# Performance work log

Hardware: AMD Instinct MI355X
Metric: run time of the kernel (lower is better)

## Reference

```python
import jax, jax.numpy as jnp
import numpy as np

ALPHA = 0.2  # LeakyReLU slope in GAT
OUT_SLOPE = 0.01  # default nn.LeakyyReLU slope for self.out
B, E, IN_DIM, HID, HEADS = 4, 2048, 32, 18, 3
DH = HID // HEADS  # per-head out dim = 6


def _leaky(x, slope):
    return jnp.where(x > 0, x, slope * x)


def _gat_head(x, adj, W, a):
    # x: [B,E,in], W: [in,dh], a: [2*dh,1]
    h = jnp.einsum('bei,id->bed', x, W)                      # [B,E,dh]
    d = h.shape[-1]
    # score[b,i,j] = leakyrelu(a . concat(h_i, h_j)) = leakyrelu(h_i.a1 + h_j.a2)
    e1 = jnp.einsum('bed,d->be', h, a[:d, 0])
    e2 = jnp.einsum('bed,d->be', h, a[d:, 0])
    score = _leaky(e1[:, :, None] + e2[:, None, :], ALPHA)   # [B,E,E]
    scores = jnp.where(adj == 1.0, score, 0.0)
    logits = jnp.where(adj > 0.0, scores, -30.0)
    att = jax.nn.softmax(logits, axis=2)                     # softmax over j
    # h_prime[b,j,d] = sum_i att[b,i,j] * h[b,i,d]  (torch sums over dim=1)
    h_prime = jnp.einsum('bij,bid->bjd', att, h)
    return jax.nn.elu(h_prime)  # concat=True -> elu


def _gat_multihead(x, adj, Ws, As):
    # Ws: [H,in,dh], As: [H,2*dh,1]
    outs = jax.vmap(lambda W, a: _gat_head(x, adj, W, a))(Ws, As)  # [H,B,E,dh]
    H, b, e, d = outs.shape
    return jnp.moveaxis(outs, 0, 2).reshape(b, e, H * d)  # concat heads last-dim


def _gcn(x, adj2d, W, b):
    return adj2d @ (x @ W) + b


def setup_inputs() -> dict:
    key = jax.random.key(0)
    ks = jax.random.split(key, 16)
    node_input = jax.random.normal(ks[0], (B, E, IN_DIM), jnp.float32)
    uv_filed = jax.random.normal(ks[1], (B, E, IN_DIM), jnp.float32)
    adj = jax.random.randint(ks[2], (B, E, E), 0, 2).astype(jnp.float32)
    s = 0.1
    Wt1 = jax.random.normal(ks[3], (HEADS, IN_DIM, DH), jnp.float32) * s
    at1 = jax.random.normal(ks[4], (HEADS, 2 * DH, 1), jnp.float32) * s
    Wt2 = jax.random.normal(ks[5], (HEADS, IN_DIM, DH), jnp.float32) * s
    at2 = jax.random.normal(ks[6], (HEADS, 2 * DH, 1), jnp.float32) * s
    Wg1 = jax.random.normal(ks[7], (HID, 16), jnp.float32) * s
    bg1 = jnp.zeros((16,), jnp.float32)
    Wg2 = jax.random.normal(ks[8], (16, 2), jnp.float32) * s
    bg2 = jnp.zeros((2,), jnp.float32)
    Wo1 = jax.random.normal(ks[9], (HID, 16), jnp.float32) * s
    bo1 = jnp.zeros((16,), jnp.float32)
    Wo2 = jax.random.normal(ks[10], (16, 2), jnp.float32) * s
    bo2 = jnp.zeros((2,), jnp.float32)
    return dict(node_input=node_input, uv_filed=uv_filed, adj=adj,
                Wt1=Wt1, at1=at1, Wt2=Wt2, at2=at2,
                Wg1=Wg1, bg1=bg1, Wg2=Wg2, bg2=bg2,
                Wo1=Wo1, bo1=bo1, Wo2=Wo2, bo2=bo2)


def reference(node_input, uv_filed, adj, Wt1, at1, Wt2, at2,
              Wg1, bg1, Wg2, bg2, Wo1, bo1, Wo2, bo2):
    h = _gat_multihead(node_input, adj, Wt1, at1)  # [B,E,18]
    o = _gat_multihead(uv_filed, adj, Wt2, at2)    # [B,E,18]
    a0 = adj[0]
    Y = jax.nn.relu(_gcn(h[0], a0, Wg1, bg1))
    O = jax.nn.relu(_gcn(o[0], a0, Wo1, bo1))
    Y = _gcn(Y, a0, Wg2, bg2)
    O = _gcn(O, a0, Wo2, bo2)
    return (jax.nn.log_softmax(Y, axis=1), _leaky(O, OUT_SLOPE))
```

## Files before the change

### kernel.cpp

```cpp
#include <hip/hip_runtime.h>
#include <hip/hip_bf16.h>


__global__ __launch_bounds__(256) void k0_bitmask(
    const float* __restrict__ adj0, unsigned int* __restrict__ bm) {
  int lane = threadIdx.x & 63, w = threadIdx.x >> 6;
  int row = blockIdx.x * 4 + w;
  const float* arow = adj0 + (size_t)row * 2048;
#pragma unroll 4
  for (int it = 0; it < 32; ++it) {
    float v = arow[it * 64 + lane];
    unsigned long long mask = __ballot(v == 1.0f);
    if (lane == 0) bm[row * 64 + it * 2] = (unsigned int)mask;
    else if (lane == 32) bm[row * 64 + it * 2 + 1] = (unsigned int)(mask >> 32);
  }
}

__global__ __launch_bounds__(256) void k1_features(
    const float* __restrict__ node, const float* __restrict__ uv,
    const float* __restrict__ Wt1, const float* __restrict__ at1,
    const float* __restrict__ Wt2, const float* __restrict__ at2,
    float* __restrict__ hcol, float* __restrict__ pack1, float* __restrict__ pack2) {
  __shared__ float sW[192];
  __shared__ float sA[12];
  int b = blockIdx.x;
  int g = b / 24;
  int h = (b / 8) % 3;
  int e = (b % 8) * 256 + threadIdx.x;
  const float* W = (g ? Wt2 : Wt1) + h * 192;
  const float* A = (g ? at2 : at1) + h * 12;
  const float* x = (g ? uv : node) + e * 32;
  if (threadIdx.x < 192) sW[threadIdx.x] = W[threadIdx.x];
  if (threadIdx.x < 12) sA[threadIdx.x] = A[threadIdx.x];
  __syncthreads();
  float xv[32];
#pragma unroll
  for (int i = 0; i < 32; ++i) xv[i] = x[i];
  float hv[6];
#pragma unroll
  for (int d = 0; d < 6; ++d) hv[d] = 0.f;
#pragma unroll
  for (int i = 0; i < 32; ++i)
#pragma unroll
    for (int d = 0; d < 6; ++d) hv[d] += xv[i] * sW[i * 6 + d];
  float e1 = 0.f, e2 = 0.f;
#pragma unroll
  for (int d = 0; d < 6; ++d) {
    e1 += hv[d] * sA[d];
    e2 += hv[d] * sA[6 + d];
  }
  int c = g * 3 + h;
#pragma unroll
  for (int d = 0; d < 6; ++d) hcol[(c * 6 + d) * 2048 + e] = hv[d];
  pack1[c * 2048 + e] = e1;
  pack1[(6 + c) * 2048 + e] = __expf(e1);
  pack1[(12 + c) * 2048 + e] = __expf(0.2f * e1);
  pack2[c * 2048 + e] = e2;
  pack2[(6 + c) * 2048 + e] = __expf(e2);
  pack2[(12 + c) * 2048 + e] = __expf(0.2f * e2);
}

__global__ __launch_bounds__(384) void k2_rowsum(
    const unsigned int* __restrict__ bm, const float* __restrict__ pack1,
    const float* __restrict__ pack2, float* __restrict__ invrs) {
  int tid = threadIdx.x;
  int c = tid >> 6, lane = tid & 63;
  int i0 = blockIdx.x * 8;
  const float4* p2_4 = (const float4*)pack2;
  float e1r[8], p1r[8], q1r[8], sum[8];
#pragma unroll
  for (int r = 0; r < 8; ++r) {
    e1r[r] = pack1[c * 2048 + i0 + r];
    p1r[r] = pack1[(6 + c) * 2048 + i0 + r];
    q1r[r] = pack1[(12 + c) * 2048 + i0 + r];
    sum[r] = 0.f;
  }
  int sh = (lane & 7) * 4;
#pragma unroll
  for (int it = 0; it < 8; ++it) {
    int j4 = it * 64 + lane;
    float4 e2 = p2_4[c * 512 + j4];
    float4 p2 = p2_4[(6 + c) * 512 + j4];
    float4 q2 = p2_4[(12 + c) * 512 + j4];
    int wbase = it * 8 + (lane >> 3);
    float abx, aby, abz, abw;
#pragma unroll
    for (int r = 0; r < 8; ++r) {
      unsigned int wd = bm[(i0 + r) * 64 + wbase] >> sh;
      { float e = e1r[r] + e2.x; bool p = e > 0.f;
        abx = (p ? p1r[r] : q1r[r]) * (p ? p2.x : q2.x); }
      { float e = e1r[r] + e2.y; bool p = e > 0.f;
        aby = (p ? p1r[r] : q1r[r]) * (p ? p2.y : q2.y); }
      { float e = e1r[r] + e2.z; bool p = e > 0.f;
        abz = (p ? p1r[r] : q1r[r]) * (p ? p2.z : q2.z); }
      { float e = e1r[r] + e2.w; bool p = e > 0.f;
        abw = (p ? p1r[r] : q1r[r]) * (p ? p2.w : q2.w); }
      float s = ((wd & 1u) ? abx : 0.f) + ((wd & 2u) ? aby : 0.f) +
                ((wd & 4u) ? abz : 0.f) + ((wd & 8u) ? abw : 0.f);
      sum[r] += s;
    }
  }
#pragma unroll
  for (int r = 0; r < 8; ++r) {
#pragma unroll
    for (int off = 32; off > 0; off >>= 1) sum[r] += __shfl_down(sum[r], off);
  }
  if (lane == 0) {
#pragma unroll
    for (int r = 0; r < 8; ++r) invrs[c * 2048 + i0 + r] = 1.0f / sum[r];
  }
}

__global__ __launch_bounds__(384) void k3_hprime(
    const unsigned int* __restrict__ bm, const float* __restrict__ hcol,
    const float* __restrict__ pack1, const float* __restrict__ pack2,
    const float* __restrict__ invrs, float* __restrict__ hp_part) {
  __shared__ float4 sPack[6 * 64];
  __shared__ float sHS[6 * 64 * 8];
  __shared__ unsigned int sM[64 * 4];
  float4* sHS4 = (float4*)sHS;
  int tid = threadIdx.x;
  int c6 = tid >> 6, jl = tid & 63;
  int j0 = blockIdx.x * 128;
  int jA = j0 + jl, jB = jA + 64;
  float e2A = pack2[c6 * 2048 + jA];
  float p2A = pack2[(6 + c6) * 2048 + jA];
  float q2A = pack2[(12 + c6) * 2048 + jA];
  float e2B = pack2[c6 * 2048 + jB];
  float p2B = pack2[(6 + c6) * 2048 + jB];
  float q2B = pack2[(12 + c6) * 2048 + jB];
  float aA0 = 0.f, aA1 = 0.f, aA2 = 0.f, aA3 = 0.f, aA4 = 0.f, aA5 = 0.f;
  float aB0 = 0.f, aB1 = 0.f, aB2 = 0.f, aB3 = 0.f, aB4 = 0.f, aB5 = 0.f;
  int hi = jl >> 5;
  int shj = jl & 31;
  int ibeg = blockIdx.y * 128;
  for (int i0 = ibeg; i0 < ibeg + 128; i0 += 64) {
    __syncthreads();
    {
      int cc = c6, ii = jl;
      float e1 = pack1[cc * 2048 + i0 + ii];
      float p1 = pack1[(6 + cc) * 2048 + i0 + ii];
      float q1 = pack1[(12 + cc) * 2048 + i0 + ii];
      sPack[cc * 64 + ii] = make_float4(e1, p1, q1, 0.f);
      float iv = invrs[cc * 2048 + i0 + ii];
#pragma unroll
      for (int d = 0; d < 6; ++d)
        sHS[(cc * 64 + ii) * 8 + d] = hcol[(cc * 6 + d) * 2048 + i0 + ii] * iv;
      sHS[(cc * 64 + ii) * 8 + 6] = 0.f;
      sHS[(cc * 64 + ii) * 8 + 7] = 0.f;
    }
    if (tid < 256) sM[tid] = bm[(size_t)(i0 + (tid >> 2)) * 64 + (j0 >> 5) + (tid & 3)];
    __syncthreads();
#pragma unroll 8
    for (int ii = 0; ii < 64; ++ii) {
      float4 pk = sPack[c6 * 64 + ii];
      float4 h0 = sHS4[(c6 * 64 + ii) * 2];
      float4 h1 = sHS4[(c6 * 64 + ii) * 2 + 1];
      unsigned int wdA = sM[ii * 4 + hi];
      unsigned int wdB = sM[ii * 4 + 2 + hi];
      {
        float e = pk.x + e2A; bool p = e > 0.f;
        float ab = (p ? pk.y : pk.z) * (p ? p2A : q2A);
        float wgt = ((wdA >> shj) & 1u) ? ab : 0.f;
        aA0 += wgt * h0.x; aA1 += wgt * h0.y; aA2 += wgt * h0.z;
        aA3 += wgt * h0.w; aA4 += wgt * h1.x; aA5 += wgt * h1.y;
      }
      {
        float e = pk.x + e2B; bool p = e > 0.f;
        float ab = (p ? pk.y : pk.z) * (p ? p2B : q2B);
        float wgt = ((wdB >> shj) & 1u) ? ab : 0.f;
        aB0 += wgt * h0.x; aB1 += wgt * h0.y; aB2 += wgt * h0.z;
        aB3 += wgt * h0.w; aB4 += wgt * h1.x; aB5 += wgt * h1.y;
      }
    }
  }
  float* hp = hp_part + (size_t)blockIdx.y * 73728;
  int kb = c6 * 6;
  hp[(kb + 0) * 2048 + jA] = aA0;
  hp[(kb + 1) * 2048 + jA] = aA1;
  hp[(kb + 2) * 2048 + jA] = aA2;
  hp[(kb + 3) * 2048 + jA] = aA3;
  hp[(kb + 4) * 2048 + jA] = aA4;
  hp[(kb + 5) * 2048 + jA] = aA5;
  hp[(kb + 0) * 2048 + jB] = aB0;
  hp[(kb + 1) * 2048 + jB] = aB1;
  hp[(kb + 2) * 2048 + jB] = aB2;
  hp[(kb + 3) * 2048 + jB] = aB3;
  hp[(kb + 4) * 2048 + jB] = aB4;
  hp[(kb + 5) * 2048 + jB] = aB5;
}

__global__ __launch_bounds__(256) void k4_T(
    const float* __restrict__ hp_part, const float* __restrict__ Wg1,
    const float* __restrict__ Wo1, float* __restrict__ T) {
  __shared__ float sHP[16 * 37];
  __shared__ float sWg[288], sWo[288];
  int tid = threadIdx.x;
  int j0 = blockIdx.x * 16;
  for (int idx = tid; idx < 288; idx += 256) {
    sWg[idx] = Wg1[idx];
    sWo[idx] = Wo1[idx];
  }
  for (int idx = tid; idx < 576; idx += 256) {
    int r = idx >> 4, jl = idx & 15;
    float s = 0.f;
#pragma unroll
    for (int sp = 0; sp < 16; ++sp)
      s += hp_part[(size_t)sp * 73728 + r * 2048 + j0 + jl];
    sHP[jl * 37 + r] = s;
  }
  __syncthreads();
  int jl = tid & 15, wq = tid >> 4;
  int gat = wq >> 3;
  int c0 = (wq & 7) * 2;
  const float* Wp = gat ? sWo : sWg;
  float a0 = 0.f, a1 = 0.f;
#pragma unroll
  for (int r = 0; r < 18; ++r) {
    float x = sHP[jl * 37 + gat * 18 + r];
    float hc = x > 0.f ? x : __expf(x) - 1.f;
    a0 += hc * Wp[r * 16 + c0];
    a1 += hc * Wp[r * 16 + c0 + 1];
  }
  T[(j0 + jl) * 32 + gat * 16 + c0] = a0;
  T[(j0 + jl) * 32 + gat * 16 + c0 + 1] = a1;
}

__global__ __launch_bounds__(256) void k5_gcn1(
    const unsigned int* __restrict__ bm, const float* __restrict__ T,
    float* __restrict__ Craw_part) {
  __shared__ unsigned int sM[64 * 4];
  __shared__ float4 sT4[128 * 8];
  const float4* T4 = (const float4*)T;
  int tid = threadIdx.x;
  int rl = tid & 31, cg = tid >> 5;
  int i0 = blockIdx.x * 64;
  int k0 = blockIdx.y * 128;
  if (tid < 256) sM[tid] = bm[(size_t)(i0 + (tid >> 2)) * 64 + (k0 >> 5) + (tid & 3)];
  for (int idx = tid; idx < 1024; idx += 256) sT4[idx] = T4[k0 * 8 + idx];
  __syncthreads();
  float a0x = 0.f, a0y = 0.f, a0z = 0.f, a0w = 0.f;
  float a1x = 0.f, a1y = 0.f, a1z = 0.f, a1w = 0.f;
#pragma unroll
  for (int wi = 0; wi < 4; ++wi) {
    unsigned int wA = sM[rl * 4 + wi];
    unsigned int wB = sM[(rl + 32) * 4 + wi];
#pragma unroll 16
    for (int kb = 0; kb < 32; ++kb) {
      float4 t = sT4[(wi * 32 + kb) * 8 + cg];
      float mA = (float)((wA >> kb) & 1u);
      float mB = (float)((wB >> kb) & 1u);
      a0x += mA * t.x; a0y += mA * t.y; a0z += mA * t.z; a0w += mA * t.w;
      a1x += mB * t.x; a1y += mB * t.y; a1z += mB * t.z; a1w += mB * t.w;
    }
  }
  float* base = Craw_part + (size_t)blockIdx.y * 65536;
  *(float4*)&base[(i0 + rl) * 32 + cg * 4] = make_float4(a0x, a0y, a0z, a0w);
  *(float4*)&base[(i0 + rl + 32) * 32 + cg * 4] = make_float4(a1x, a1y, a1z, a1w);
}

__global__ __launch_bounds__(256) void k6_T2(
    const float* __restrict__ Craw_part, const float* __restrict__ bg1,
    const float* __restrict__ Wg2, const float* __restrict__ bo1,
    const float* __restrict__ Wo2, float* __restrict__ T2) {
  int tid = threadIdx.x;
  int wave = tid >> 6, lane = tid & 63;
  int j = blockIdx.x * 8 + wave * 2 + (lane >> 5);
  int cl = lane & 31;
  int gat = cl >> 4, cc = cl & 15;
  float x = 0.f;
#pragma unroll
  for (int sp = 0; sp < 16; ++sp) x += Craw_part[(size_t)sp * 65536 + j * 32 + cl];
  x += gat ? bo1[cc] : bg1[cc];
  x = x > 0.f ? x : 0.f;
  float wa = gat ? Wo2[cc * 2 + 0] : Wg2[cc * 2 + 0];
  float wb = gat ? Wo2[cc * 2 + 1] : Wg2[cc * 2 + 1];
  float pa = x * wa, pb = x * wb;
#pragma unroll
  for (int m = 8; m > 0; m >>= 1) {
    pa += __shfl_xor(pa, m);
    pb += __shfl_xor(pb, m);
  }
  if (cc == 0) {
    T2[j * 4 + gat * 2 + 0] = pa;
    T2[j * 4 + gat * 2 + 1] = pb;
  }
}

__global__ __launch_bounds__(256) void k7_final(
    const unsigned int* __restrict__ bm, const float* __restrict__ T2,
    const float* __restrict__ bg2, const float* __restrict__ bo2,
    float* __restrict__ out) {
  int tid = threadIdx.x;
  int lane = tid & 63, w = tid >> 6;
  int r = blockIdx.x * 4 + w;
  const float4* T24 = (const float4*)T2;
  float4 acc = make_float4(0.f, 0.f, 0.f, 0.f);
  int sh = lane & 31;
#pragma unroll 8
  for (int it = 0; it < 32; ++it) {
    int k = it * 64 + lane;
    unsigned int wd = bm[r * 64 + it * 2 + (lane >> 5)];
    float m = (float)((wd >> sh) & 1u);
    float4 t = T24[k];
    acc.x += m * t.x;
    acc.y += m * t.y;
    acc.z += m * t.z;
    acc.w += m * t.w;
  }
#pragma unroll
  for (int off = 32; off > 0; off >>= 1) {
    acc.x += __shfl_down(acc.x, off);
    acc.y += __shfl_down(acc.y, off);
    acc.z += __shfl_down(acc.z, off);
    acc.w += __shfl_down(acc.w, off);
  }
  if (lane == 0) {
    float y0 = acc.x + bg2[0], y1 = acc.y + bg2[1];
    float m = fmaxf(y0, y1);
    float ls = m + logf(__expf(y0 - m) + __expf(y1 - m));
    out[r * 2 + 0] = y0 - ls;
    out[r * 2 + 1] = y1 - ls;
    float o0 = acc.z + bo2[0], o1 = acc.w + bo2[1];
    out[4096 + r * 2 + 0] = o0 > 0.f ? o0 : 0.01f * o0;
    out[4096 + r * 2 + 1] = o1 > 0.f ? o1 : 0.01f * o1;
  }
}

extern "C" void kernel_launch(void* const* d_in, const int* in_sizes, int n_in,
                              void* d_out, int out_size, void* d_ws, size_t ws_size,
                              hipStream_t stream) {
  const float* node = (const float*)d_in[0];
  const float* uv = (const float*)d_in[1];
  const float* adj = (const float*)d_in[2];
  const float* Wt1 = (const float*)d_in[3];
  const float* at1 = (const float*)d_in[4];
  const float* Wt2 = (const float*)d_in[5];
  const float* at2 = (const float*)d_in[6];
  const float* Wg1 = (const float*)d_in[7];
  const float* bg1 = (const float*)d_in[8];
  const float* Wg2 = (const float*)d_in[9];
  const float* bg2 = (const float*)d_in[10];
  const float* Wo1 = (const float*)d_in[11];
  const float* bo1 = (const float*)d_in[12];
  const float* Wo2 = (const float*)d_in[13];
  const float* bo2 = (const float*)d_in[14];
  float* ws = (float*)d_ws;
  float* hcol = ws;
  float* pack1 = ws + 73728;
  float* pack2 = ws + 110592;
  float* invrs = ws + 147456;
  float* T = ws + 159744;
  float* T2 = ws + 225280;
  unsigned int* bm = (unsigned int*)(ws + 233472);
  float* hp_part = ws + 364544;
  float* Craw_part = ws + 1544192;
  float* out = (float*)d_out;

  k0_bitmask<<<512, 256, 0, stream>>>(adj, bm);
  k1_features<<<48, 256, 0, stream>>>(node, uv, Wt1, at1, Wt2, at2, hcol, pack1, pack2);
  k2_rowsum<<<256, 384, 0, stream>>>(bm, pack1, pack2, invrs);
  k3_hprime<<<dim3(16, 16), 384, 0, stream>>>(bm, hcol, pack1, pack2, invrs, hp_part);
  k4_T<<<128, 256, 0, stream>>>(hp_part, Wg1, Wo1, T);
  k5_gcn1<<<dim3(32, 16), 256, 0, stream>>>(bm, T, Craw_part);
  k6_T2<<<256, 256, 0, stream>>>(Craw_part, bg1, Wg2, bo1, Wo2, T2);
  k7_final<<<512, 256, 0, stream>>>(bm, T2, bg2, bo2, out);
}
```

Measured before the change: 183.6 us.

## Merge bitmask and feature kernels, precompute scaled h, drop LDS staging in hprime

```diff
diff --git a/kernel.cpp b/kernel.cpp
--- a/kernel.cpp
+++ b/kernel.cpp
@@ -2,31 +2,32 @@
 #include <hip/hip_bf16.h>
 
 
-__global__ __launch_bounds__(256) void k0_bitmask(
-    const float* __restrict__ adj0, unsigned int* __restrict__ bm) {
-  int lane = threadIdx.x & 63, w = threadIdx.x >> 6;
-  int row = blockIdx.x * 4 + w;
-  const float* arow = adj0 + (size_t)row * 2048;
-#pragma unroll 4
-  for (int it = 0; it < 32; ++it) {
-    float v = arow[it * 64 + lane];
-    unsigned long long mask = __ballot(v == 1.0f);
-    if (lane == 0) bm[row * 64 + it * 2] = (unsigned int)mask;
-    else if (lane == 32) bm[row * 64 + it * 2 + 1] = (unsigned int)(mask >> 32);
-  }
-}
-
-__global__ __launch_bounds__(256) void k1_features(
+__global__ __launch_bounds__(256) void k01(
+    const float* __restrict__ adj0, unsigned int* __restrict__ bm,
     const float* __restrict__ node, const float* __restrict__ uv,
     const float* __restrict__ Wt1, const float* __restrict__ at1,
     const float* __restrict__ Wt2, const float* __restrict__ at2,
-    float* __restrict__ hcol, float* __restrict__ pack1, float* __restrict__ pack2) {
+    float* __restrict__ hcol, float4* __restrict__ pk1q, float* __restrict__ pack2) {
+  int b = blockIdx.x;
+  if (b < 512) {
+    int lane = threadIdx.x & 63, w = threadIdx.x >> 6;
+    int row = b * 4 + w;
+    const float* arow = adj0 + (size_t)row * 2048;
+#pragma unroll 4
+    for (int it = 0; it < 32; ++it) {
+      float v = arow[it * 64 + lane];
+      unsigned long long mask = __ballot(v == 1.0f);
+      if (lane == 0) bm[row * 64 + it * 2] = (unsigned int)mask;
+      else if (lane == 32) bm[row * 64 + it * 2 + 1] = (unsigned int)(mask >> 32);
+    }
+    return;
+  }
   __shared__ float sW[192];
   __shared__ float sA[12];
-  int b = blockIdx.x;
-  int g = b / 24;
-  int h = (b / 8) % 3;
-  int e = (b % 8) * 256 + threadIdx.x;
+  int fb = b - 512;
+  int g = fb / 24;
+  int h = (fb / 8) % 3;
+  int e = (fb % 8) * 256 + threadIdx.x;
   const float* W = (g ? Wt2 : Wt1) + h * 192;
   const float* A = (g ? at2 : at1) + h * 12;
   const float* x = (g ? uv : node) + e * 32;
@@ -52,27 +53,25 @@
   int c = g * 3 + h;
 #pragma unroll
   for (int d = 0; d < 6; ++d) hcol[(c * 6 + d) * 2048 + e] = hv[d];
-  pack1[c * 2048 + e] = e1;
-  pack1[(6 + c) * 2048 + e] = __expf(e1);
-  pack1[(12 + c) * 2048 + e] = __expf(0.2f * e1);
+  pk1q[c * 2048 + e] = make_float4(e1, __expf(e1), __expf(0.2f * e1), 0.f);
   pack2[c * 2048 + e] = e2;
   pack2[(6 + c) * 2048 + e] = __expf(e2);
   pack2[(12 + c) * 2048 + e] = __expf(0.2f * e2);
 }
 
-__global__ __launch_bounds__(384) void k2_rowsum(
-    const unsigned int* __restrict__ bm, const float* __restrict__ pack1,
-    const float* __restrict__ pack2, float* __restrict__ invrs) {
+__global__ __launch_bounds__(384) void k2_rowsum_hs(
+    const unsigned int* __restrict__ bm, const float4* __restrict__ pk1q,
+    const float* __restrict__ pack2, const float* __restrict__ hcol,
+    float* __restrict__ hs8) {
   int tid = threadIdx.x;
   int c = tid >> 6, lane = tid & 63;
-  int i0 = blockIdx.x * 8;
+  int i0 = blockIdx.x * 4;
   const float4* p2_4 = (const float4*)pack2;
-  float e1r[8], p1r[8], q1r[8], sum[8];
-#pragma unroll
-  for (int r = 0; r < 8; ++r) {
-    e1r[r] = pack1[c * 2048 + i0 + r];
-    p1r[r] = pack1[(6 + c) * 2048 + i0 + r];
-    q1r[r] = pack1[(12 + c) * 2048 + i0 + r];
+  float e1r[4], p1r[4], q1r[4], sum[4];
+#pragma unroll
+  for (int r = 0; r < 4; ++r) {
+    float4 pq = pk1q[c * 2048 + i0 + r];
+    e1r[r] = pq.x; p1r[r] = pq.y; q1r[r] = pq.z;
     sum[r] = 0.f;
   }
   int sh = (lane & 7) * 4;
@@ -85,7 +84,7 @@
     int wbase = it * 8 + (lane >> 3);
     float abx, aby, abz, abw;
 #pragma unroll
-    for (int r = 0; r < 8; ++r) {
+    for (int r = 0; r < 4; ++r) {
       unsigned int wd = bm[(i0 + r) * 64 + wbase] >> sh;
       { float e = e1r[r] + e2.x; bool p = e > 0.f;
         abx = (p ? p1r[r] : q1r[r]) * (p ? p2.x : q2.x); }
@@ -101,27 +100,29 @@
     }
   }
 #pragma unroll
-  for (int r = 0; r < 8; ++r) {
+  for (int r = 0; r < 4; ++r) {
 #pragma unroll
     for (int off = 32; off > 0; off >>= 1) sum[r] += __shfl_down(sum[r], off);
   }
-  if (lane == 0) {
-#pragma unroll
-    for (int r = 0; r < 8; ++r) invrs[c * 2048 + i0 + r] = 1.0f / sum[r];
+  float s0 = __shfl(sum[0], 0), s1 = __shfl(sum[1], 0);
+  float s2 = __shfl(sum[2], 0), s3 = __shfl(sum[3], 0);
+  if (lane < 32) {
+    int r = lane >> 3, d = lane & 7;
+    float sv = (r == 0) ? s0 : (r == 1) ? s1 : (r == 2) ? s2 : s3;
+    float v = 0.f;
+    if (d < 6) v = hcol[(c * 6 + d) * 2048 + i0 + r] * (1.0f / sv);
+    hs8[((size_t)c * 2048 + i0 + r) * 8 + d] = v;
   }
 }
 
 __global__ __launch_bounds__(384) void k3_hprime(
-    const unsigned int* __restrict__ bm, const float* __restrict__ hcol,
-    const float* __restrict__ pack1, const float* __restrict__ pack2,
-    const float* __restrict__ invrs, float* __restrict__ hp_part) {
-  __shared__ float4 sPack[6 * 64];
-  __shared__ float sHS[6 * 64 * 8];
-  __shared__ unsigned int sM[64 * 4];
-  float4* sHS4 = (float4*)sHS;
+    const unsigned int* __restrict__ bm, const float4* __restrict__ pk1q,
+    const float* __restrict__ pack2, const float4* __restrict__ hs8,
+    float* __restrict__ hp_part) {
   int tid = threadIdx.x;
   int c6 = tid >> 6, jl = tid & 63;
   int j0 = blockIdx.x * 128;
+  int i0 = blockIdx.y * 64;
   int jA = j0 + jl, jB = jA + 64;
   float e2A = pack2[c6 * 2048 + jA];
   float p2A = pack2[(6 + c6) * 2048 + jA];
@@ -133,45 +134,30 @@
   float aB0 = 0.f, aB1 = 0.f, aB2 = 0.f, aB3 = 0.f, aB4 = 0.f, aB5 = 0.f;
   int hi = jl >> 5;
   int shj = jl & 31;
-  int ibeg = blockIdx.y * 128;
-  for (int i0 = ibeg; i0 < ibeg + 128; i0 += 64) {
-    __syncthreads();
+  const float4* pk1 = pk1q + c6 * 2048;
+  const float4* hs = hs8 + (size_t)c6 * 2048 * 2;
+  const unsigned int* bmA = bm + (size_t)i0 * 64 + (j0 >> 5) + hi;
+#pragma unroll 4
+  for (int ii = 0; ii < 64; ++ii) {
+    int irow = i0 + ii;
+    float4 pk = pk1[irow];
+    float4 h0 = hs[irow * 2];
+    float4 h1 = hs[irow * 2 + 1];
+    unsigned int wdA = bmA[ii * 64];
+    unsigned int wdB = bmA[ii * 64 + 2];
     {
-      int cc = c6, ii = jl;
-      float e1 = pack1[cc * 2048 + i0 + ii];
-      float p1 = pack1[(6 + cc) * 2048 + i0 + ii];
-      float q1 = pack1[(12 + cc) * 2048 + i0 + ii];
-      sPack[cc * 64 + ii] = make_float4(e1, p1, q1, 0.f);
-      float iv = invrs[cc * 2048 + i0 + ii];
-#pragma unroll
-      for (int d = 0; d < 6; ++d)
-        sHS[(cc * 64 + ii) * 8 + d] = hcol[(cc * 6 + d) * 2048 + i0 + ii] * iv;
-      sHS[(cc * 64 + ii) * 8 + 6] = 0.f;
-      sHS[(cc * 64 + ii) * 8 + 7] = 0.f;
-    }
-    if (tid < 256) sM[tid] = bm[(size_t)(i0 + (tid >> 2)) * 64 + (j0 >> 5) + (tid & 3)];
-    __syncthreads();
-#pragma unroll 8
-    for (int ii = 0; ii < 64; ++ii) {
-      float4 pk = sPack[c6 * 64 + ii];
-      float4 h0 = sHS4[(c6 * 64 + ii) * 2];
-      float4 h1 = sHS4[(c6 * 64 + ii) * 2 + 1];
-      unsigned int wdA = sM[ii * 4 + hi];
-      unsigned int wdB = sM[ii * 4 + 2 + hi];
-      {
-        float e = pk.x + e2A; bool p = e > 0.f;
-        float ab = (p ? pk.y : pk.z) * (p ? p2A : q2A);
-        float wgt = ((wdA >> shj) & 1u) ? ab : 0.f;
-        aA0 += wgt * h0.x; aA1 += wgt * h0.y; aA2 += wgt * h0.z;
-        aA3 += wgt * h0.w; aA4 += wgt * h1.x; aA5 += wgt * h1.y;
-      }
-      {
-        float e = pk.x + e2B; bool p = e > 0.f;
-        float ab = (p ? pk.y : pk.z) * (p ? p2B : q2B);
-        float wgt = ((wdB >> shj) & 1u) ? ab : 0.f;
-        aB0 += wgt * h0.x; aB1 += wgt * h0.y; aB2 += wgt * h0.z;
-        aB3 += wgt * h0.w; aB4 += wgt * h1.x; aB5 += wgt * h1.y;
-      }
+      float e = pk.x + e2A; bool p = e > 0.f;
+      float ab = (p ? pk.y : pk.z) * (p ? p2A : q2A);
+      float w = ((wdA >> shj) & 1u) ? ab : 0.f;
+      aA0 += w * h0.x; aA1 += w * h0.y; aA2 += w * h0.z;
+      aA3 += w * h0.w; aA4 += w * h1.x; aA5 += w * h1.y;
+    }
+    {
+      float e = pk.x + e2B; bool p = e > 0.f;
+      float ab = (p ? pk.y : pk.z) * (p ? p2B : q2B);
+      float w = ((wdB >> shj) & 1u) ? ab : 0.f;
+      aB0 += w * h0.x; aB1 += w * h0.y; aB2 += w * h0.z;
+      aB3 += w * h0.w; aB4 += w * h1.x; aB5 += w * h1.y;
     }
   }
   float* hp = hp_part + (size_t)blockIdx.y * 73728;
@@ -193,37 +179,31 @@
 __global__ __launch_bounds__(256) void k4_T(
     const float* __restrict__ hp_part, const float* __restrict__ Wg1,
     const float* __restrict__ Wo1, float* __restrict__ T) {
-  __shared__ float sHP[16 * 37];
+  __shared__ float sHP[8 * 37];
   __shared__ float sWg[288], sWo[288];
   int tid = threadIdx.x;
-  int j0 = blockIdx.x * 16;
+  int j0 = blockIdx.x * 8;
   for (int idx = tid; idx < 288; idx += 256) {
     sWg[idx] = Wg1[idx];
     sWo[idx] = Wo1[idx];
   }
-  for (int idx = tid; idx < 576; idx += 256) {
-    int r = idx >> 4, jl = idx & 15;
+  for (int idx = tid; idx < 288; idx += 256) {
+    int r = idx >> 3, jl = idx & 7;
     float s = 0.f;
 #pragma unroll
-    for (int sp = 0; sp < 16; ++sp)
+    for (int sp = 0; sp < 32; ++sp)
       s += hp_part[(size_t)sp * 73728 + r * 2048 + j0 + jl];
-    sHP[jl * 37 + r] = s;
+    sHP[jl * 37 + r] = s > 0.f ? s : __expf(s) - 1.f;
   }
   __syncthreads();
-  int jl = tid & 15, wq = tid >> 4;
-  int gat = wq >> 3;
-  int c0 = (wq & 7) * 2;
+  int jl = tid >> 5, col = tid & 31;
+  int gat = col >> 4, cc = col & 15;
   const float* Wp = gat ? sWo : sWg;
-  float a0 = 0.f, a1 = 0.f;
-#pragma unroll
-  for (int r = 0; r < 18; ++r) {
-    float x = sHP[jl * 37 + gat * 18 + r];
-    float hc = x > 0.f ? x : __expf(x) - 1.f;
-    a0 += hc * Wp[r * 16 + c0];
-    a1 += hc * Wp[r * 16 + c0 + 1];
-  }
-  T[(j0 + jl) * 32 + gat * 16 + c0] = a0;
-  T[(j0 + jl) * 32 + gat * 16 + c0 + 1] = a1;
+  float a = 0.f;
+#pragma unroll
+  for (int r = 0; r < 18; ++r)
+    a += sHP[jl * 37 + gat * 18 + r] * Wp[r * 16 + cc];
+  T[(j0 + jl) * 32 + col] = a;
 }
 
 __global__ __launch_bounds__(256) void k5_gcn1(
@@ -236,7 +216,7 @@
   int rl = tid & 31, cg = tid >> 5;
   int i0 = blockIdx.x * 64;
   int k0 = blockIdx.y * 128;
-  if (tid < 256) sM[tid] = bm[(size_t)(i0 + (tid >> 2)) * 64 + (k0 >> 5) + (tid & 3)];
+  sM[tid] = bm[(size_t)(i0 + (tid >> 2)) * 64 + (k0 >> 5) + (tid & 3)];
   for (int idx = tid; idx < 1024; idx += 256) sT4[idx] = T4[k0 * 8 + idx];
   __syncthreads();
   float a0x = 0.f, a0y = 0.f, a0z = 0.f, a0w = 0.f;
@@ -347,21 +327,21 @@
   const float* bo2 = (const float*)d_in[14];
   float* ws = (float*)d_ws;
   float* hcol = ws;
-  float* pack1 = ws + 73728;
-  float* pack2 = ws + 110592;
-  float* invrs = ws + 147456;
-  float* T = ws + 159744;
-  float* T2 = ws + 225280;
-  unsigned int* bm = (unsigned int*)(ws + 233472);
-  float* hp_part = ws + 364544;
-  float* Craw_part = ws + 1544192;
+  float* pack2 = ws + 73728;
+  float4* pk1q = (float4*)(ws + 110592);
+  float* hs8 = ws + 159744;
+  float* T = ws + 258048;
+  float* T2 = ws + 323584;
+  unsigned int* bm = (unsigned int*)(ws + 331776);
+  float* hp_part = ws + 462848;
+  float* Craw_part = ws + 2822144;
   float* out = (float*)d_out;
 
-  k0_bitmask<<<512, 256, 0, stream>>>(adj, bm);
-  k1_features<<<48, 256, 0, stream>>>(node, uv, Wt1, at1, Wt2, at2, hcol, pack1, pack2);
-  k2_rowsum<<<256, 384, 0, stream>>>(bm, pack1, pack2, invrs);
-  k3_hprime<<<dim3(16, 16), 384, 0, stream>>>(bm, hcol, pack1, pack2, invrs, hp_part);
-  k4_T<<<128, 256, 0, stream>>>(hp_part, Wg1, Wo1, T);
+  k01<<<560, 256, 0, stream>>>(adj, bm, node, uv, Wt1, at1, Wt2, at2,
+                               hcol, pk1q, pack2);
+  k2_rowsum_hs<<<512, 384, 0, stream>>>(bm, pk1q, pack2, hcol, hs8);
+  k3_hprime<<<dim3(16, 32), 384, 0, stream>>>(bm, pk1q, pack2, (const float4*)hs8, hp_part);
+  k4_T<<<256, 256, 0, stream>>>(hp_part, Wg1, Wo1, T);
   k5_gcn1<<<dim3(32, 16), 256, 0, stream>>>(bm, T, Craw_part);
   k6_T2<<<256, 256, 0, stream>>>(Craw_part, bg1, Wg2, bo1, Wo2, T2);
   k7_final<<<512, 256, 0, stream>>>(bm, T2, bg2, bo2, out);
```

Result: slower. 200.9 us (+9.4%).
